# Performance work log

Hardware: AMD Instinct MI355X
Metric: run time of the kernel (lower is better)

Reference implementation:

```python
import jax, jax.numpy as jnp
import numpy as np

N = 50000      # nodes
E = 800000     # edges (avg degree 16)
IN = 128       # in_dim == hidden_dim*num_heads so residuals fire
D = 32         # hidden_dim (per-head)
H = 4          # num_heads
OUT = 64       # out_dim (final layer has 1 head)
NEG_SLOPE = 0.2
LN_EPS = 1e-5


def setup_inputs() -> dict:
    key = jax.random.key(0)
    ks = jax.random.split(key, 16)
    rn = lambda k, s: jax.random.normal(k, s, jnp.float32) * 0.05
    return {
        "features": jax.random.normal(ks[0], (N, IN), jnp.float32),
        "edge_weight": jax.random.uniform(ks[1], (E,), jnp.float32),
        "src": jax.random.randint(ks[2], (E,), 0, N),
        "dst": jax.random.randint(ks[3], (E,), 0, N),
        "W0": rn(ks[4], (IN, H * D)), "al0": rn(ks[5], (H, D)), "ar0": rn(ks[6], (H, D)), "lam0": jnp.float32(1.0),
        "W1": rn(ks[7], (H * D, H * D)), "al1": rn(ks[8], (H, D)), "ar1": rn(ks[9], (H, D)), "lam1": jnp.float32(1.0),
        "W2": rn(ks[10], (H * D, OUT)), "al2": rn(ks[11], (1, OUT)), "ar2": rn(ks[12], (1, OUT)), "lam2": jnp.float32(1.0),
        "g0": jnp.ones((H * D,), jnp.float32), "b0": jnp.zeros((H * D,), jnp.float32),
        "g1": jnp.ones((H * D,), jnp.float32), "b1": jnp.zeros((H * D,), jnp.float32),
    }


def _gat_layer(h, W, al, ar, lam, src, dst, ew):
    n = h.shape[0]
    heads, d = al.shape
    ft = (h @ W).reshape(n, heads, d)                      # [N,H,D]
    el = jnp.sum(ft * al[None], axis=-1)                   # [N,H]
    er = jnp.sum(ft * ar[None], axis=-1)                   # [N,H]
    e = el[src] + er[dst] + lam * ew[:, None]              # [E,H] u_add_v + weight bias
    e = jax.nn.leaky_relu(e, NEG_SLOPE)
    # edge softmax over incoming edges of each dst node
    m = jax.ops.segment_max(e, dst, num_segments=n)        # [N,H]
    ex = jnp.exp(e - m[dst])
    s = jax.ops.segment_sum(ex, dst, num_segments=n)       # [N,H]
    a = ex / s[dst]                                        # [E,H]
    # u_mul_e + sum aggregation
    msg = ft[src] * a[:, :, None]                          # [E,H,D]
    return jax.ops.segment_sum(msg, dst, num_segments=n)   # [N,H,D]


def _layer_norm(x, g, b):
    mu = jnp.mean(x, axis=-1, keepdims=True)
    var = jnp.mean((x - mu) ** 2, axis=-1, keepdims=True)
    return (x - mu) * jax.lax.rsqrt(var + LN_EPS) * g + b


def _forward(features, edge_weight, src, dst,
             W0, al0, ar0, lam0, W1, al1, ar1, lam1, W2, al2, ar2, lam2,
             g0, b0, g1, b1):
    n = features.shape[0]
    h = features
    # layer 0
    h1 = _gat_layer(h, W0, al0, ar0, lam0, src, dst, edge_weight)
    h1 = jax.nn.elu(h1).reshape(n, -1)
    h1 = _layer_norm(h1, g0, b0)
    if h1.shape == h.shape:
        h1 = h1 + h
    # layer 1
    h2 = _gat_layer(h1, W1, al1, ar1, lam1, src, dst, edge_weight)
    h2 = jax.nn.elu(h2).reshape(n, -1)
    h2 = _layer_norm(h2, g1, b1)
    h2 = h2 + h1
    # layer 2 (single head, no activation)
    out = _gat_layer(h2, W2, al2, ar2, lam2, src, dst, edge_weight).reshape(n, -1)
    return out


def reference(features, edge_weight, src, dst,
              W0, al0, ar0, lam0, W1, al1, ar1, lam1, W2, al2, ar2, lam2,
              g0, b0, g1, b1):
    # eval mode: dropout off and _add_noise is identity, so noisy == clean
    h_clean = _forward(features, edge_weight, src, dst,
                       W0, al0, ar0, lam0, W1, al1, ar1, lam1, W2, al2, ar2, lam2,
                       g0, b0, g1, b1)
    return (h_clean, h_clean)
```

## Files before the change

kernel.cpp:

```cpp
#include <hip/hip_runtime.h>

#define NEG_SLOPE 0.2f
#define LN_EPS 1e-5f

typedef __attribute__((ext_vector_type(8))) short bf16x8;
typedef __attribute__((ext_vector_type(4))) float f32x4;

__device__ inline unsigned short f2bf(float f) {
    unsigned u = __float_as_uint(f);
    unsigned r = u + 0x7FFFu + ((u >> 16) & 1u);
    return (unsigned short)(r >> 16);
}

__device__ inline void unpack8(uint4 u, float* f) {
    f[0] = __uint_as_float(u.x << 16);
    f[1] = __uint_as_float(u.x & 0xFFFF0000u);
    f[2] = __uint_as_float(u.y << 16);
    f[3] = __uint_as_float(u.y & 0xFFFF0000u);
    f[4] = __uint_as_float(u.z << 16);
    f[5] = __uint_as_float(u.z & 0xFFFF0000u);
    f[6] = __uint_as_float(u.w << 16);
    f[7] = __uint_as_float(u.w & 0xFFFF0000u);
}


__global__ __launch_bounds__(256) void zero_wt_kernel(
    uint4* __restrict__ z, int nz, int ZB,
    const float* __restrict__ W0, const float* __restrict__ W1,
    const float* __restrict__ W2, unsigned short* __restrict__ Wt0,
    unsigned short* __restrict__ Wt1, unsigned short* __restrict__ Wt2) {
    int bid = blockIdx.x;
    if (bid < ZB) {
        int base = bid * 1024 + threadIdx.x;
        #pragma unroll
        for (int j = 0; j < 4; ++j) {
            int idx = base + j * 256;
            if (idx < nz) z[idx] = make_uint4(0, 0, 0, 0);
        }
    } else {
        int row = (bid - ZB) * 2 + (threadIdx.x >> 7);
        int k = threadIdx.x & 127;
        if (row < 128) {
            Wt0[row * 128 + k] = f2bf(W0[k * 128 + row]);
        } else if (row < 256) {
            int c = row - 128;
            Wt1[c * 128 + k] = f2bf(W1[k * 128 + c]);
        } else {
            int c = row - 256;
            Wt2[c * 128 + k] = f2bf(W2[k * 64 + c]);
        }
    }
}


__global__ __launch_bounds__(256) void hist_gemm0(
    const int* __restrict__ dst, int* __restrict__ counts, int* __restrict__ rank,
    int E, int RB, const float* __restrict__ Ap, const unsigned short* __restrict__ Wt,
    const float* __restrict__ al, const float* __restrict__ ar,
    unsigned short* __restrict__ ftb, float* __restrict__ el,
    float* __restrict__ er, int n) {
    constexpr int LDA = 136;
    constexpr int NT = 8, H = 4, D = 32;
    __shared__ unsigned short As[64 * LDA];
    __shared__ unsigned short Ws[NT * 16 * LDA];
    int t = threadIdx.x;
    if (blockIdx.x < RB) {
        int i = blockIdx.x * 256 + t;
        if (i < E) rank[i] = atomicAdd(&counts[dst[i] * 16], 1);
        return;
    }
    int row0 = (blockIdx.x - RB) * 64;

    const float4* A4 = (const float4*)Ap;
    #pragma unroll
    for (int j = 0; j < 8; ++j) {
        int idx = t + j * 256;
        int r = idx >> 5;
        int c4 = idx & 31;
        int row = row0 + r;
        float4 v = (row < n) ? A4[(size_t)row * 32 + c4] : make_float4(0.f, 0.f, 0.f, 0.f);
        unsigned p0 = (unsigned)f2bf(v.x) | ((unsigned)f2bf(v.y) << 16);
        unsigned p1 = (unsigned)f2bf(v.z) | ((unsigned)f2bf(v.w) << 16);
        *(uint2*)&As[r * LDA + c4 * 4] = make_uint2(p0, p1);
    }
    const uint4* Wg = (const uint4*)Wt;
    #pragma unroll
    for (int j = 0; j < NT; ++j) {
        int idx = t + j * 256;
        int r = idx >> 4;
        int c8 = idx & 15;
        *(uint4*)&Ws[r * LDA + c8 * 8] = Wg[idx];
    }
    __syncthreads();

    int w = t >> 6, lane = t & 63;
    int m = lane & 15, q = lane >> 4;
    f32x4 acc[NT] = {};
    const unsigned short* ap = &As[(w * 16 + m) * LDA + q * 8];
    #pragma unroll
    for (int kk = 0; kk < 4; ++kk) {
        bf16x8 a = *(const bf16x8*)(ap + kk * 32);
        #pragma unroll
        for (int nt = 0; nt < NT; ++nt) {
            bf16x8 b = *(const bf16x8*)&Ws[(nt * 16 + m) * LDA + kk * 32 + q * 8];
            acc[nt] = __builtin_amdgcn_mfma_f32_16x16x32_bf16(a, b, acc[nt], 0, 0, 0);
        }
    }

    float alv[NT], arv[NT];
    #pragma unroll
    for (int nt = 0; nt < NT; ++nt) {
        alv[nt] = al[nt * 16 + m];
        arv[nt] = ar[nt * 16 + m];
    }

    int orow = row0 + w * 16 + q * 4;
    #pragma unroll
    for (int r = 0; r < 4; ++r) {
        int row = orow + r;
        float pl[H] = {}, pr[H] = {};
        #pragma unroll
        for (int nt = 0; nt < NT; ++nt) {
            int h = (nt * 16) / D;
            pl[h] = fmaf(acc[nt][r], alv[nt], pl[h]);
            pr[h] = fmaf(acc[nt][r], arv[nt], pr[h]);
        }
        #pragma unroll
        for (int off = 1; off < 16; off <<= 1) {
            #pragma unroll
            for (int h = 0; h < H; ++h) {
                pl[h] += __shfl_xor(pl[h], off, 64);
                pr[h] += __shfl_xor(pr[h], off, 64);
            }
        }
        if (row < n) {
            #pragma unroll
            for (int nt = 0; nt < NT; ++nt)
                ftb[(size_t)row * 128 + nt * 16 + m] = f2bf(acc[nt][r]);
            if (m < H) {
                float vl = pl[0], vr = pr[0];
                #pragma unroll
                for (int h = 1; h < H; ++h)
                    if (m == h) { vl = pl[h]; vr = pr[h]; }
                el[row * H + m] = vl;
                er[row * H + m] = vr;
            }
        }
    }
}


__global__ __launch_bounds__(256) void scan1_kernel(const int* __restrict__ counts,
                                                    int* __restrict__ bsum,
                                                    int* __restrict__ dhist, int n) {
    __shared__ int lds[256];
    __shared__ int hbin[64];
    int t = threadIdx.x;
    if (t < 64) hbin[t] = 0;
    int i = blockIdx.x * 256 + t;
    int c = (i < n) ? counts[i * 16] : 0;
    lds[t] = c;
    __syncthreads();
    if (i < n) atomicAdd(&hbin[63 - (c < 63 ? c : 63)], 1);
    for (int off = 128; off > 0; off >>= 1) {
        int v = (t < off) ? lds[t + off] : 0;
        __syncthreads();
        if (t < off) lds[t] += v;
        __syncthreads();
    }
    if (t == 0) bsum[blockIdx.x] = lds[0];
    if (t < 64) {
        int h = hbin[t];
        if (h) atomicAdd(&dhist[t], h);
    }
}


__global__ __launch_bounds__(256) void scan3_kernel(const int* __restrict__ counts,
                                                    const int* __restrict__ bsum,
                                                    int* __restrict__ rowptr,
                                                    const int* __restrict__ dhist,
                                                    int* __restrict__ dbase,
                                                    int n, int E, int nscan) {
    __shared__ int lds[256];
    int t = threadIdx.x;
    lds[t] = (t < nscan) ? bsum[t] : 0;
    __syncthreads();
    for (int off = 1; off < 256; off <<= 1) {
        int v = (t >= off) ? lds[t - off] : 0;
        __syncthreads();
        lds[t] += v;
        __syncthreads();
    }
    int boff = (blockIdx.x > 0) ? lds[blockIdx.x - 1] : 0;
    __syncthreads();
    int i = blockIdx.x * 256 + t;
    int c = (i < n) ? counts[i * 16] : 0;
    lds[t] = c;
    __syncthreads();
    for (int off = 1; off < 256; off <<= 1) {
        int v = (t >= off) ? lds[t - off] : 0;
        __syncthreads();
        lds[t] += v;
        __syncthreads();
    }
    if (i < n) rowptr[i] = boff + lds[t] - c;
    if (i == n) rowptr[n] = E;
    if (blockIdx.x == 0 && t < 64) {
        int v = dhist[t];
        int x = v;
        #pragma unroll
        for (int off = 1; off < 64; off <<= 1) {
            int u = __shfl_up(x, off, 64);
            if (t >= off) x += u;
        }
        dbase[t] = x - v;
    }
}


__global__ __launch_bounds__(256) void place_kernel(
    const int* __restrict__ src, const int* __restrict__ dst,
    const float* __restrict__ ew, const int* __restrict__ rowptr,
    const int* __restrict__ rank, unsigned* __restrict__ edge_p,
    const int* __restrict__ dbase, int* __restrict__ dcount,
    int* __restrict__ perm, int E, int EB, int N) {
    __shared__ int lbin[64];
    __shared__ int lbase[64];
    int bid = blockIdx.x;
    int t = threadIdx.x;
    if (bid < EB) {
        int i = bid * 256 + t;
        if (i < E) {
            int p = rowptr[dst[i]] + rank[i];
            edge_p[p] = ((unsigned)f2bf(ew[i]) << 16) | (unsigned)src[i];
        }
    } else {
        if (t < 64) lbin[t] = 0;
        __syncthreads();
        int nidx = (bid - EB) * 256 + t;
        bool valid = nidx < N;
        int key = 0, myoff = 0;
        if (valid) {
            int deg = rowptr[nidx + 1] - rowptr[nidx];
            key = 63 - (deg < 63 ? deg : 63);
            myoff = atomicAdd(&lbin[key], 1);
        }
        __syncthreads();
        if (t < 64) lbase[t] = lbin[t] ? atomicAdd(&dcount[t], lbin[t]) : 0;
        __syncthreads();
        if (valid) perm[dbase[key] + lbase[key] + myoff] = nidx;
    }
}


__device__ inline void accum8(float* ax, uint4 u, float p) {
    ax[0] = fmaf(p, __uint_as_float(u.x << 16), ax[0]);
    ax[1] = fmaf(p, __uint_as_float(u.x & 0xFFFF0000u), ax[1]);
    ax[2] = fmaf(p, __uint_as_float(u.y << 16), ax[2]);
    ax[3] = fmaf(p, __uint_as_float(u.y & 0xFFFF0000u), ax[3]);
    ax[4] = fmaf(p, __uint_as_float(u.z << 16), ax[4]);
    ax[5] = fmaf(p, __uint_as_float(u.z & 0xFFFF0000u), ax[5]);
    ax[6] = fmaf(p, __uint_as_float(u.w << 16), ax[6]);
    ax[7] = fmaf(p, __uint_as_float(u.w & 0xFFFF0000u), ax[7]);
}

__device__ inline void accum4(float* ax, uint2 u, float p) {
    ax[0] = fmaf(p, __uint_as_float(u.x << 16), ax[0]);
    ax[1] = fmaf(p, __uint_as_float(u.x & 0xFFFF0000u), ax[1]);
    ax[2] = fmaf(p, __uint_as_float(u.y << 16), ax[2]);
    ax[3] = fmaf(p, __uint_as_float(u.y & 0xFFFF0000u), ax[3]);
}

template <int K>
__device__ inline void agg_batch(const uint4* __restrict__ ftb4,
                                 const float* __restrict__ el, unsigned ev, int j,
                                 int li, int head, float erv, float lam, float* ax,
                                 float& s) {
    unsigned ee[K];
    uint4 uu[K];
    float ll[K];
    #pragma unroll
    for (int k = 0; k < K; ++k) ee[k] = __shfl(ev, j + k, 16);
    #pragma unroll
    for (int k = 0; k < K; ++k) {
        unsigned sn = ee[k] & 0xFFFFu;
        uu[k] = ftb4[(size_t)sn * 16 + li];
        ll[k] = el[sn * 4 + head];
    }
    #pragma unroll
    for (int k = 0; k < K; ++k) {
        float v = ll[k] + erv + lam * __uint_as_float(ee[k] & 0xFFFF0000u);
        v = fmaxf(v, NEG_SLOPE * v);
        float p = __expf(v);
        accum8(ax, uu[k], p);
        s += p;
    }
}

template <int K>
__device__ inline void agg_batch_out(const uint2* __restrict__ ftb2,
                                     const float* __restrict__ el, unsigned ev,
                                     int j, int li, float erv, float lam, float* ax,
                                     float& s) {
    unsigned ee[K];
    uint2 uu[K];
    float ll[K];
    #pragma unroll
    for (int k = 0; k < K; ++k) ee[k] = __shfl(ev, j + k, 16);
    #pragma unroll
    for (int k = 0; k < K; ++k) {
        unsigned sn = ee[k] & 0xFFFFu;
        uu[k] = ftb2[(size_t)sn * 16 + li];
        ll[k] = el[sn];
    }
    #pragma unroll
    for (int k = 0; k < K; ++k) {
        float v = ll[k] + erv + lam * __uint_as_float(ee[k] & 0xFFFF0000u);
        v = fmaxf(v, NEG_SLOPE * v);
        float p = __expf(v);
        accum4(ax, uu[k], p);
        s += p;
    }
}


template <bool PREV32, int VER>
__global__ __launch_bounds__(256) void fused_agg_gemm(
    const int* __restrict__ rowptr, const unsigned* __restrict__ edge_p,
    const int* __restrict__ perm, const uint4* __restrict__ ftb4,
    const float* __restrict__ el_in, const float* __restrict__ er_in,
    const float* __restrict__ lam_p, const float* __restrict__ g,
    const float* __restrict__ b, const void* __restrict__ prevp,
    uint4* __restrict__ houtb, const unsigned short* __restrict__ Wt,
    const float* __restrict__ al, const float* __restrict__ ar,
    unsigned short* __restrict__ ftb_out, float* __restrict__ el_out,
    float* __restrict__ er_out, int n) {
    constexpr int LDA = 136;
    __shared__ unsigned short As[16 * LDA];
    __shared__ float red[2][4][16];
    int t = threadIdx.x;
    int node0 = blockIdx.x * 16;
    int nl = t >> 4;
    int gid = node0 + nl;
    int li = t & 15;

    if (gid < n) {
        int node = perm[gid];
        int head = li >> 2;
        float lam = lam_p[0];
        float erv = er_in[node * 4 + head];
        int s0 = rowptr[node], s1 = rowptr[node + 1];
        float ax[8] = {};
        float s = 0.f;

        for (int base = s0; base < s1; base += 16) {
            int m = s1 - base;
            if (m > 16) m = 16;
            unsigned ev = (li < m) ? edge_p[base + li] : 0u;
            int j = 0;
            for (; j + 8 <= m; j += 8)
                agg_batch<8>(ftb4, el_in, ev, j, li, head, erv, lam, ax, s);
            if (j + 4 <= m) {
                agg_batch<4>(ftb4, el_in, ev, j, li, head, erv, lam, ax, s);
                j += 4;
            }
            for (; j < m; ++j)
                agg_batch<1>(ftb4, el_in, ev, j, li, head, erv, lam, ax, s);
        }

        float inv = (s > 0.f) ? 1.f / s : 0.f;
        float x[8];
        float sum = 0.f, sq = 0.f;
        #pragma unroll
        for (int d = 0; d < 8; ++d) {
            float v = ax[d] * inv;
            v = (v > 0.f) ? v : expm1f(v);
            x[d] = v;
            sum += v;
            sq += v * v;
        }
        #pragma unroll
        for (int off = 1; off < 16; off <<= 1) {
            sum += __shfl_xor(sum, off, 16);
            sq += __shfl_xor(sq, off, 16);
        }
        float mu = sum * (1.f / 128.f);
        float var = sq * (1.f / 128.f) - mu * mu;
        float rs = rsqrtf(var + LN_EPS);

        const float4* g4 = (const float4*)g;
        const float4* b4 = (const float4*)b;
        float pv[8];
        if constexpr (PREV32) {
            const float4* p4 = (const float4*)prevp;
            #pragma unroll
            for (int h = 0; h < 2; ++h) {
                float4 v = p4[(size_t)node * 32 + li * 2 + h];
                pv[h * 4 + 0] = v.x; pv[h * 4 + 1] = v.y;
                pv[h * 4 + 2] = v.z; pv[h * 4 + 3] = v.w;
            }
        } else {
            unpack8(((const uint4*)prevp)[(size_t)node * 16 + li], pv);
        }
        float y[8];
        #pragma unroll
        for (int h = 0; h < 2; ++h) {
            float4 gv = g4[li * 2 + h];
            float4 bv = b4[li * 2 + h];
            y[h * 4 + 0] = (x[h * 4 + 0] - mu) * rs * gv.x + bv.x + pv[h * 4 + 0];
            y[h * 4 + 1] = (x[h * 4 + 1] - mu) * rs * gv.y + bv.y + pv[h * 4 + 1];
            y[h * 4 + 2] = (x[h * 4 + 2] - mu) * rs * gv.z + bv.z + pv[h * 4 + 2];
            y[h * 4 + 3] = (x[h * 4 + 3] - mu) * rs * gv.w + bv.w + pv[h * 4 + 3];
        }
        uint4 o;
        o.x = (unsigned)f2bf(y[0]) | ((unsigned)f2bf(y[1]) << 16);
        o.y = (unsigned)f2bf(y[2]) | ((unsigned)f2bf(y[3]) << 16);
        o.z = (unsigned)f2bf(y[4]) | ((unsigned)f2bf(y[5]) << 16);
        o.w = (unsigned)f2bf(y[6]) | ((unsigned)f2bf(y[7]) << 16);
        if constexpr (VER == 1) houtb[(size_t)node * 16 + li] = o;
        *(uint4*)&As[nl * LDA + li * 8] = o;
    } else {
        *(uint4*)&As[nl * LDA + li * 8] = make_uint4(0, 0, 0, 0);
    }
    __syncthreads();

    int w = t >> 6, lane = t & 63;
    int m = lane & 15, q = lane >> 4;
    if constexpr (VER == 1) {
        f32x4 acc[2] = {};
        #pragma unroll
        for (int kk = 0; kk < 4; ++kk) {
            bf16x8 a = *(const bf16x8*)&As[m * LDA + kk * 32 + q * 8];
            #pragma unroll
            for (int nt = 0; nt < 2; ++nt) {
                int col = w * 32 + nt * 16 + m;
                bf16x8 bb = *(const bf16x8*)&Wt[(size_t)col * 128 + kk * 32 + q * 8];
                acc[nt] = __builtin_amdgcn_mfma_f32_16x16x32_bf16(a, bb, acc[nt], 0, 0, 0);
            }
        }
        float alv0 = al[w * 32 + m], alv1 = al[w * 32 + 16 + m];
        float arv0 = ar[w * 32 + m], arv1 = ar[w * 32 + 16 + m];
        #pragma unroll
        for (int r = 0; r < 4; ++r) {
            int gr = node0 + q * 4 + r;
            float pl = acc[0][r] * alv0 + acc[1][r] * alv1;
            float pr = acc[0][r] * arv0 + acc[1][r] * arv1;
            #pragma unroll
            for (int off = 1; off < 16; off <<= 1) {
                pl += __shfl_xor(pl, off, 64);
                pr += __shfl_xor(pr, off, 64);
            }
            if (gr < n) {
                int row = perm[gr];
                ftb_out[(size_t)row * 128 + w * 32 + m] = f2bf(acc[0][r]);
                ftb_out[(size_t)row * 128 + w * 32 + 16 + m] = f2bf(acc[1][r]);
                if (m == 0) {
                    el_out[row * 4 + w] = pl;
                    er_out[row * 4 + w] = pr;
                }
            }
        }
    } else {
        f32x4 acc = {};
        #pragma unroll
        for (int kk = 0; kk < 4; ++kk) {
            bf16x8 a = *(const bf16x8*)&As[m * LDA + kk * 32 + q * 8];
            int col = w * 16 + m;
            bf16x8 bb = *(const bf16x8*)&Wt[(size_t)col * 128 + kk * 32 + q * 8];
            acc = __builtin_amdgcn_mfma_f32_16x16x32_bf16(a, bb, acc, 0, 0, 0);
        }
        float alv = al[w * 16 + m], arv = ar[w * 16 + m];
        #pragma unroll
        for (int r = 0; r < 4; ++r) {
            int gr = node0 + q * 4 + r;
            float pl = acc[r] * alv;
            float pr = acc[r] * arv;
            #pragma unroll
            for (int off = 1; off < 16; off <<= 1) {
                pl += __shfl_xor(pl, off, 64);
                pr += __shfl_xor(pr, off, 64);
            }
            if (gr < n) ftb_out[(size_t)perm[gr] * 64 + w * 16 + m] = f2bf(acc[r]);
            if (m == 0) {
                red[0][w][q * 4 + r] = pl;
                red[1][w][q * 4 + r] = pr;
            }
        }
        __syncthreads();
        if (t < 16) {
            int gr = node0 + t;
            if (gr < n) {
                int row = perm[gr];
                el_out[row] = red[0][0][t] + red[0][1][t] + red[0][2][t] + red[0][3][t];
                er_out[row] = red[1][0][t] + red[1][1][t] + red[1][2][t] + red[1][3][t];
            }
        }
    }
}


__global__ __launch_bounds__(256) void gat_agg_out(
    const int* __restrict__ rowptr, const unsigned* __restrict__ edge_p,
    const int* __restrict__ perm, const uint2* __restrict__ ftb2,
    const float* __restrict__ el, const float* __restrict__ er,
    const float* __restrict__ lam_p, float* __restrict__ out, int n) {
    int gid = blockIdx.x * 16 + (threadIdx.x >> 4);
    if (gid >= n) return;
    int node = perm[gid];
    int li = threadIdx.x & 15;
    float lam = lam_p[0];
    float erv = er[node];
    int s0 = rowptr[node], s1 = rowptr[node + 1];
    float ax[4] = {};
    float s = 0.f;

    for (int base = s0; base < s1; base += 16) {
        int m = s1 - base;
        if (m > 16) m = 16;
        unsigned ev = (li < m) ? edge_p[base + li] : 0u;
        int j = 0;
        for (; j + 8 <= m; j += 8)
            agg_batch_out<8>(ftb2, el, ev, j, li, erv, lam, ax, s);
        if (j + 4 <= m) {
            agg_batch_out<4>(ftb2, el, ev, j, li, erv, lam, ax, s);
            j += 4;
        }
        for (; j < m; ++j)
            agg_batch_out<1>(ftb2, el, ev, j, li, erv, lam, ax, s);
    }

    float inv = (s > 0.f) ? 1.f / s : 0.f;
    float4 y;
    y.x = ax[0] * inv;
    y.y = ax[1] * inv;
    y.z = ax[2] * inv;
    y.w = ax[3] * inv;
    ((float4*)out)[(size_t)node * 16 + li] = y;
    ((float4*)out)[(size_t)(n + node) * 16 + li] = y;
}


extern "C" void kernel_launch(void* const* d_in, const int* in_sizes, int n_in,
                              void* d_out, int out_size, void* d_ws, size_t ws_size,
                              hipStream_t stream) {
    const float* features = (const float*)d_in[0];
    const float* edge_weight = (const float*)d_in[1];
    const int* src = (const int*)d_in[2];
    const int* dst = (const int*)d_in[3];
    const float* W0 = (const float*)d_in[4];
    const float* al0 = (const float*)d_in[5];
    const float* ar0 = (const float*)d_in[6];
    const float* lam0 = (const float*)d_in[7];
    const float* W1 = (const float*)d_in[8];
    const float* al1 = (const float*)d_in[9];
    const float* ar1 = (const float*)d_in[10];
    const float* lam1 = (const float*)d_in[11];
    const float* W2 = (const float*)d_in[12];
    const float* al2 = (const float*)d_in[13];
    const float* ar2 = (const float*)d_in[14];
    const float* lam2 = (const float*)d_in[15];
    const float* g0 = (const float*)d_in[16];
    const float* b0 = (const float*)d_in[17];
    const float* g1 = (const float*)d_in[18];
    const float* b1 = (const float*)d_in[19];

    const int N = in_sizes[0] / 128;
    const int E = in_sizes[1];

    char* w = (char*)d_ws;
    size_t o = 0;
    auto carve = [&](size_t bytes) {
        char* p = w + o;
        o += (bytes + 255) & ~(size_t)255;
        return p;
    };
    int* counts = (int*)carve((size_t)N * 64);
    int* dhist = (int*)carve(256);
    int* dcount = (int*)carve(256);
    int* rowptr = (int*)carve((size_t)(N + 1) * 4);
    int* bsum = (int*)carve(256 * 4);
    int* dbase = (int*)carve(256);
    int* rank = (int*)carve((size_t)E * 4);
    unsigned* edge_p = (unsigned*)carve((size_t)E * 4);
    int* perm = (int*)carve((size_t)N * 4);
    unsigned short* ftbA = (unsigned short*)carve((size_t)N * 128 * 2);
    unsigned short* ftbB = (unsigned short*)carve((size_t)N * 128 * 2);
    unsigned short* ftbC = (unsigned short*)carve((size_t)N * 64 * 2);
    unsigned short* h1 = (unsigned short*)carve((size_t)N * 128 * 2);
    float* elA = (float*)carve((size_t)N * 4 * 4);
    float* erA = (float*)carve((size_t)N * 4 * 4);
    float* elB = (float*)carve((size_t)N * 4 * 4);
    float* erB = (float*)carve((size_t)N * 4 * 4);
    float* elC = (float*)carve((size_t)N * 4);
    float* erC = (float*)carve((size_t)N * 4);
    unsigned short* Wt0 = (unsigned short*)carve(128 * 128 * 2);
    unsigned short* Wt1 = (unsigned short*)carve(128 * 128 * 2);
    unsigned short* Wt2 = (unsigned short*)carve(64 * 128 * 2);

    const int nscan = (N + 255) / 256;
    const int ngemm = (N + 63) / 64;
    const int nagg = (N + 15) / 16;
    const int RB = (E + 255) / 256;
    const int nz = N * 4 + 32;
    const int ZB = (nz + 1023) / 1024;

    zero_wt_kernel<<<ZB + 160, 256, 0, stream>>>((uint4*)counts, nz, ZB,
                                                 W0, W1, W2, Wt0, Wt1, Wt2);
    hist_gemm0<<<RB + ngemm, 256, 0, stream>>>(dst, counts, rank, E, RB,
                                               features, Wt0, al0, ar0,
                                               ftbA, elA, erA, N);
    scan1_kernel<<<nscan, 256, 0, stream>>>(counts, bsum, dhist, N);
    scan3_kernel<<<(N + 1 + 255) / 256, 256, 0, stream>>>(counts, bsum, rowptr,
                                                          dhist, dbase, N, E, nscan);
    place_kernel<<<RB + nscan, 256, 0, stream>>>(src, dst, edge_weight, rowptr, rank,
                                                 edge_p, dbase, dcount, perm, E, RB, N);
    fused_agg_gemm<true, 1><<<nagg, 256, 0, stream>>>(
        rowptr, edge_p, perm, (const uint4*)ftbA, elA, erA, lam0, g0, b0, features,
        (uint4*)h1, Wt1, al1, ar1, ftbB, elB, erB, N);
    fused_agg_gemm<false, 2><<<nagg, 256, 0, stream>>>(
        rowptr, edge_p, perm, (const uint4*)ftbB, elB, erB, lam1, g1, b1, h1,
        nullptr, Wt2, al2, ar2, ftbC, elC, erC, N);
    gat_agg_out<<<nagg, 256, 0, stream>>>(rowptr, edge_p, perm, (const uint2*)ftbC,
                                          elC, erC, lam2, (float*)d_out, N);
}
```

Measured before the change: 290.1 us.

## Store node features in degree-sorted order and coalesce GEMM output writes

```diff
diff --git a/kernel.cpp b/kernel.cpp
--- a/kernel.cpp
+++ b/kernel.cpp
@@ -24,21 +24,17 @@
 }
 
 
-__global__ __launch_bounds__(256) void zero_wt_kernel(
-    uint4* __restrict__ z, int nz, int ZB,
-    const float* __restrict__ W0, const float* __restrict__ W1,
+__global__ __launch_bounds__(256) void prep_kernel(
+    const int* __restrict__ dst, int* __restrict__ counts, int* __restrict__ rank,
+    int E, int RB, const float* __restrict__ W0, const float* __restrict__ W1,
     const float* __restrict__ W2, unsigned short* __restrict__ Wt0,
     unsigned short* __restrict__ Wt1, unsigned short* __restrict__ Wt2) {
     int bid = blockIdx.x;
-    if (bid < ZB) {
-        int base = bid * 1024 + threadIdx.x;
-        #pragma unroll
-        for (int j = 0; j < 4; ++j) {
-            int idx = base + j * 256;
-            if (idx < nz) z[idx] = make_uint4(0, 0, 0, 0);
-        }
+    if (bid < RB) {
+        int i = bid * 256 + threadIdx.x;
+        if (i < E) rank[i] = atomicAdd(&counts[dst[i] * 16], 1);
     } else {
-        int row = (bid - ZB) * 2 + (threadIdx.x >> 7);
+        int row = (bid - RB) * 2 + (threadIdx.x >> 7);
         int k = threadIdx.x & 127;
         if (row < 128) {
             Wt0[row * 128 + k] = f2bf(W0[k * 128 + row]);
@@ -53,12 +49,101 @@
 }
 
 
-__global__ __launch_bounds__(256) void hist_gemm0(
-    const int* __restrict__ dst, int* __restrict__ counts, int* __restrict__ rank,
-    int E, int RB, const float* __restrict__ Ap, const unsigned short* __restrict__ Wt,
-    const float* __restrict__ al, const float* __restrict__ ar,
-    unsigned short* __restrict__ ftb, float* __restrict__ el,
-    float* __restrict__ er, int n) {
+__global__ __launch_bounds__(256) void scan1_kernel(const int* __restrict__ counts,
+                                                    int* __restrict__ bsum,
+                                                    int* __restrict__ dhist, int n) {
+    __shared__ int lds[256];
+    __shared__ int hbin[64];
+    int t = threadIdx.x;
+    if (t < 64) hbin[t] = 0;
+    int i = blockIdx.x * 256 + t;
+    int c = (i < n) ? counts[i * 16] : 0;
+    lds[t] = c;
+    __syncthreads();
+    if (i < n) atomicAdd(&hbin[63 - (c < 63 ? c : 63)], 1);
+    for (int off = 128; off > 0; off >>= 1) {
+        int v = (t < off) ? lds[t + off] : 0;
+        __syncthreads();
+        if (t < off) lds[t] += v;
+        __syncthreads();
+    }
+    if (t == 0) bsum[blockIdx.x] = lds[0];
+    if (t < 64) {
+        int h = hbin[t];
+        if (h) atomicAdd(&dhist[t], h);
+    }
+}
+
+
+__global__ __launch_bounds__(256) void scan3_kernel(
+    const int* __restrict__ counts, const int* __restrict__ bsum,
+    int* __restrict__ rowptr, const int* __restrict__ dhist,
+    int* __restrict__ dcount, int* __restrict__ perm, int* __restrict__ ipos,
+    int n, int E, int nscan) {
+    __shared__ int lds[256];
+    __shared__ int lbin[64];
+    __shared__ int lbase[64];
+    __shared__ int dbs[64];
+    int t = threadIdx.x;
+    if (t < 64) lbin[t] = 0;
+    lds[t] = (t < nscan) ? bsum[t] : 0;
+    __syncthreads();
+    for (int off = 1; off < 256; off <<= 1) {
+        int v = (t >= off) ? lds[t - off] : 0;
+        __syncthreads();
+        lds[t] += v;
+        __syncthreads();
+    }
+    int boff = (blockIdx.x > 0) ? lds[blockIdx.x - 1] : 0;
+    __syncthreads();
+    int i = blockIdx.x * 256 + t;
+    int c = (i < n) ? counts[i * 16] : 0;
+    lds[t] = c;
+    __syncthreads();
+    for (int off = 1; off < 256; off <<= 1) {
+        int v = (t >= off) ? lds[t - off] : 0;
+        __syncthreads();
+        lds[t] += v;
+        __syncthreads();
+    }
+    if (i < n) rowptr[i] = boff + lds[t] - c;
+    if (i == n) rowptr[n] = E;
+    int key = 0, off2 = 0;
+    bool valid = i < n;
+    if (valid) {
+        key = 63 - (c < 63 ? c : 63);
+        off2 = atomicAdd(&lbin[key], 1);
+    }
+    __syncthreads();
+    if (t < 64) {
+        int v = dhist[t];
+        int x = v;
+        #pragma unroll
+        for (int o = 1; o < 64; o <<= 1) {
+            int u = __shfl_up(x, o, 64);
+            if (t >= o) x += u;
+        }
+        dbs[t] = x - v;
+        lbase[t] = lbin[t] ? atomicAdd(&dcount[t], lbin[t]) : 0;
+    }
+    __syncthreads();
+    if (valid) {
+        int slot = dbs[key] + lbase[key] + off2;
+        perm[slot] = i;
+        ipos[i] = slot;
+    }
+}
+
+
+__global__ __launch_bounds__(256) void place_gemm0(
+    const int* __restrict__ src, const int* __restrict__ dst,
+    const float* __restrict__ ew, const int* __restrict__ rowptr,
+    const int* __restrict__ rank, const int* __restrict__ ipos,
+    unsigned* __restrict__ edge_p, int E, int RB,
+    const float* __restrict__ Ap, const int* __restrict__ perm,
+    const unsigned short* __restrict__ Wt, const float* __restrict__ al,
+    const float* __restrict__ ar, unsigned short* __restrict__ ftb,
+    float* __restrict__ el, float* __restrict__ er, int n) {
     constexpr int LDA = 136;
     constexpr int NT = 8, H = 4, D = 32;
     __shared__ unsigned short As[64 * LDA];
@@ -66,7 +151,10 @@
     int t = threadIdx.x;
     if (blockIdx.x < RB) {
         int i = blockIdx.x * 256 + t;
-        if (i < E) rank[i] = atomicAdd(&counts[dst[i] * 16], 1);
+        if (i < E) {
+            int p = rowptr[dst[i]] + rank[i];
+            edge_p[p] = ((unsigned)f2bf(ew[i]) << 16) | (unsigned)ipos[src[i]];
+        }
         return;
     }
     int row0 = (blockIdx.x - RB) * 64;
@@ -77,8 +165,9 @@
         int idx = t + j * 256;
         int r = idx >> 5;
         int c4 = idx & 31;
-        int row = row0 + r;
-        float4 v = (row < n) ? A4[(size_t)row * 32 + c4] : make_float4(0.f, 0.f, 0.f, 0.f);
+        int grow = row0 + r;
+        float4 v = make_float4(0.f, 0.f, 0.f, 0.f);
+        if (grow < n) v = A4[(size_t)perm[grow] * 32 + c4];
         unsigned p0 = (unsigned)f2bf(v.x) | ((unsigned)f2bf(v.y) << 16);
         unsigned p1 = (unsigned)f2bf(v.z) | ((unsigned)f2bf(v.w) << 16);
         *(uint2*)&As[r * LDA + c4 * 4] = make_uint2(p0, p1);
@@ -146,110 +235,6 @@
                 er[row * H + m] = vr;
             }
         }
-    }
-}
-
-
-__global__ __launch_bounds__(256) void scan1_kernel(const int* __restrict__ counts,
-                                                    int* __restrict__ bsum,
-                                                    int* __restrict__ dhist, int n) {
-    __shared__ int lds[256];
-    __shared__ int hbin[64];
-    int t = threadIdx.x;
-    if (t < 64) hbin[t] = 0;
-    int i = blockIdx.x * 256 + t;
-    int c = (i < n) ? counts[i * 16] : 0;
-    lds[t] = c;
-    __syncthreads();
-    if (i < n) atomicAdd(&hbin[63 - (c < 63 ? c : 63)], 1);
-    for (int off = 128; off > 0; off >>= 1) {
-        int v = (t < off) ? lds[t + off] : 0;
-        __syncthreads();
-        if (t < off) lds[t] += v;
-        __syncthreads();
-    }
-    if (t == 0) bsum[blockIdx.x] = lds[0];
-    if (t < 64) {
-        int h = hbin[t];
-        if (h) atomicAdd(&dhist[t], h);
-    }
-}
-
-
-__global__ __launch_bounds__(256) void scan3_kernel(const int* __restrict__ counts,
-                                                    const int* __restrict__ bsum,
-                                                    int* __restrict__ rowptr,
-                                                    const int* __restrict__ dhist,
-                                                    int* __restrict__ dbase,
-                                                    int n, int E, int nscan) {
-    __shared__ int lds[256];
-    int t = threadIdx.x;
-    lds[t] = (t < nscan) ? bsum[t] : 0;
-    __syncthreads();
-    for (int off = 1; off < 256; off <<= 1) {
-        int v = (t >= off) ? lds[t - off] : 0;
-        __syncthreads();
-        lds[t] += v;
-        __syncthreads();
-    }
-    int boff = (blockIdx.x > 0) ? lds[blockIdx.x - 1] : 0;
-    __syncthreads();
-    int i = blockIdx.x * 256 + t;
-    int c = (i < n) ? counts[i * 16] : 0;
-    lds[t] = c;
-    __syncthreads();
-    for (int off = 1; off < 256; off <<= 1) {
-        int v = (t >= off) ? lds[t - off] : 0;
-        __syncthreads();
-        lds[t] += v;
-        __syncthreads();
-    }
-    if (i < n) rowptr[i] = boff + lds[t] - c;
-    if (i == n) rowptr[n] = E;
-    if (blockIdx.x == 0 && t < 64) {
-        int v = dhist[t];
-        int x = v;
-        #pragma unroll
-        for (int off = 1; off < 64; off <<= 1) {
-            int u = __shfl_up(x, off, 64);
-            if (t >= off) x += u;
-        }
-        dbase[t] = x - v;
-    }
-}
-
-
-__global__ __launch_bounds__(256) void place_kernel(
-    const int* __restrict__ src, const int* __restrict__ dst,
-    const float* __restrict__ ew, const int* __restrict__ rowptr,
-    const int* __restrict__ rank, unsigned* __restrict__ edge_p,
-    const int* __restrict__ dbase, int* __restrict__ dcount,
-    int* __restrict__ perm, int E, int EB, int N) {
-    __shared__ int lbin[64];
-    __shared__ int lbase[64];
-    int bid = blockIdx.x;
-    int t = threadIdx.x;
-    if (bid < EB) {
-        int i = bid * 256 + t;
-        if (i < E) {
-            int p = rowptr[dst[i]] + rank[i];
-            edge_p[p] = ((unsigned)f2bf(ew[i]) << 16) | (unsigned)src[i];
-        }
-    } else {
-        if (t < 64) lbin[t] = 0;
-        __syncthreads();
-        int nidx = (bid - EB) * 256 + t;
-        bool valid = nidx < N;
-        int key = 0, myoff = 0;
-        if (valid) {
-            int deg = rowptr[nidx + 1] - rowptr[nidx];
-            key = 63 - (deg < 63 ? deg : 63);
-            myoff = atomicAdd(&lbin[key], 1);
-        }
-        __syncthreads();
-        if (t < 64) lbase[t] = lbin[t] ? atomicAdd(&dcount[t], lbin[t]) : 0;
-        __syncthreads();
-        if (valid) perm[dbase[key] + lbase[key] + myoff] = nidx;
     }
 }
 
@@ -346,11 +331,11 @@
     int li = t & 15;
 
     if (gid < n) {
-        int node = perm[gid];
         int head = li >> 2;
         float lam = lam_p[0];
-        float erv = er_in[node * 4 + head];
-        int s0 = rowptr[node], s1 = rowptr[node + 1];
+        float erv = er_in[gid * 4 + head];
+        int tnode = perm[gid];
+        int s0 = rowptr[tnode], s1 = rowptr[tnode + 1];
         float ax[8] = {};
         float s = 0.f;
 
@@ -396,12 +381,12 @@
             const float4* p4 = (const float4*)prevp;
             #pragma unroll
             for (int h = 0; h < 2; ++h) {
-                float4 v = p4[(size_t)node * 32 + li * 2 + h];
+                float4 v = p4[(size_t)tnode * 32 + li * 2 + h];
                 pv[h * 4 + 0] = v.x; pv[h * 4 + 1] = v.y;
                 pv[h * 4 + 2] = v.z; pv[h * 4 + 3] = v.w;
             }
         } else {
-            unpack8(((const uint4*)prevp)[(size_t)node * 16 + li], pv);
+            unpack8(((const uint4*)prevp)[(size_t)gid * 16 + li], pv);
         }
         float y[8];
         #pragma unroll
@@ -418,7 +403,7 @@
         o.y = (unsigned)f2bf(y[2]) | ((unsigned)f2bf(y[3]) << 16);
         o.z = (unsigned)f2bf(y[4]) | ((unsigned)f2bf(y[5]) << 16);
         o.w = (unsigned)f2bf(y[6]) | ((unsigned)f2bf(y[7]) << 16);
-        if constexpr (VER == 1) houtb[(size_t)node * 16 + li] = o;
+        if constexpr (VER == 1) houtb[(size_t)gid * 16 + li] = o;
         *(uint4*)&As[nl * LDA + li * 8] = o;
     } else {
         *(uint4*)&As[nl * LDA + li * 8] = make_uint4(0, 0, 0, 0);
@@ -443,7 +428,8 @@
         float arv0 = ar[w * 32 + m], arv1 = ar[w * 32 + 16 + m];
         #pragma unroll
         for (int r = 0; r < 4; ++r) {
-            int gr = node0 + q * 4 + r;
+            int srow = q * 4 + r;
+            int gr = node0 + srow;
             float pl = acc[0][r] * alv0 + acc[1][r] * alv1;
             float pr = acc[0][r] * arv0 + acc[1][r] * arv1;
             #pragma unroll
@@ -451,15 +437,24 @@
                 pl += __shfl_xor(pl, off, 64);
                 pr += __shfl_xor(pr, off, 64);
             }
-            if (gr < n) {
-                int row = perm[gr];
-                ftb_out[(size_t)row * 128 + w * 32 + m] = f2bf(acc[0][r]);
-                ftb_out[(size_t)row * 128 + w * 32 + 16 + m] = f2bf(acc[1][r]);
-                if (m == 0) {
-                    el_out[row * 4 + w] = pl;
-                    er_out[row * 4 + w] = pr;
-                }
-            }
+            if (m == 0 && gr < n) {
+                el_out[gr * 4 + w] = pl;
+                er_out[gr * 4 + w] = pr;
+            }
+        }
+        __syncthreads();
+        #pragma unroll
+        for (int r = 0; r < 4; ++r) {
+            int srow = q * 4 + r;
+            As[srow * LDA + w * 32 + m] = f2bf(acc[0][r]);
+            As[srow * LDA + w * 32 + 16 + m] = f2bf(acc[1][r]);
+        }
+        __syncthreads();
+        {
+            int row = t >> 4, c8 = t & 15;
+            int gr = node0 + row;
+            if (gr < n)
+                ((uint4*)ftb_out)[(size_t)gr * 16 + c8] = *(const uint4*)&As[row * LDA + c8 * 8];
         }
     } else {
         f32x4 acc = {};
@@ -473,7 +468,7 @@
         float alv = al[w * 16 + m], arv = ar[w * 16 + m];
         #pragma unroll
         for (int r = 0; r < 4; ++r) {
-            int gr = node0 + q * 4 + r;
+            int srow = q * 4 + r;
             float pl = acc[r] * alv;
             float pr = acc[r] * arv;
             #pragma unroll
@@ -481,19 +476,29 @@
                 pl += __shfl_xor(pl, off, 64);
                 pr += __shfl_xor(pr, off, 64);
             }
-            if (gr < n) ftb_out[(size_t)perm[gr] * 64 + w * 16 + m] = f2bf(acc[r]);
             if (m == 0) {
-                red[0][w][q * 4 + r] = pl;
-                red[1][w][q * 4 + r] = pr;
-            }
-        }
-        __syncthreads();
+                red[0][w][srow] = pl;
+                red[1][w][srow] = pr;
+            }
+        }
+        __syncthreads();
+        #pragma unroll
+        for (int r = 0; r < 4; ++r) {
+            int srow = q * 4 + r;
+            As[srow * LDA + w * 16 + m] = f2bf(acc[r]);
+        }
+        __syncthreads();
+        if (t < 128) {
+            int row = t >> 3, c8 = t & 7;
+            int gr = node0 + row;
+            if (gr < n)
+                ((uint4*)ftb_out)[(size_t)gr * 8 + c8] = *(const uint4*)&As[row * LDA + c8 * 8];
+        }
         if (t < 16) {
             int gr = node0 + t;
             if (gr < n) {
-                int row = perm[gr];
-                el_out[row] = red[0][0][t] + red[0][1][t] + red[0][2][t] + red[0][3][t];
-                er_out[row] = red[1][0][t] + red[1][1][t] + red[1][2][t] + red[1][3][t];
+                el_out[gr] = red[0][0][t] + red[0][1][t] + red[0][2][t] + red[0][3][t];
+                er_out[gr] = red[1][0][t] + red[1][1][t] + red[1][2][t] + red[1][3][t];
             }
         }
     }
@@ -507,11 +512,11 @@
     const float* __restrict__ lam_p, float* __restrict__ out, int n) {
     int gid = blockIdx.x * 16 + (threadIdx.x >> 4);
     if (gid >= n) return;
-    int node = perm[gid];
+    int tnode = perm[gid];
     int li = threadIdx.x & 15;
     float lam = lam_p[0];
-    float erv = er[node];
-    int s0 = rowptr[node], s1 = rowptr[node + 1];
+    float erv = er[gid];
+    int s0 = rowptr[tnode], s1 = rowptr[tnode + 1];
     float ax[4] = {};
     float s = 0.f;
 
@@ -536,8 +541,8 @@
     y.y = ax[1] * inv;
     y.z = ax[2] * inv;
     y.w = ax[3] * inv;
-    ((float4*)out)[(size_t)node * 16 + li] = y;
-    ((float4*)out)[(size_t)(n + node) * 16 + li] = y;
+    ((float4*)out)[(size_t)tnode * 16 + li] = y;
+    ((float4*)out)[(size_t)(n + tnode) * 16 + li] = y;
 }
 
 
@@ -580,10 +585,10 @@
     int* dcount = (int*)carve(256);
     int* rowptr = (int*)carve((size_t)(N + 1) * 4);
     int* bsum = (int*)carve(256 * 4);
-    int* dbase = (int*)carve(256);
     int* rank = (int*)carve((size_t)E * 4);
     unsigned* edge_p = (unsigned*)carve((size_t)E * 4);
     int* perm = (int*)carve((size_t)N * 4);
+    int* ipos = (int*)carve((size_t)N * 4);
     unsigned short* ftbA = (unsigned short*)carve((size_t)N * 128 * 2);
     unsigned short* ftbB = (unsigned short*)carve((size_t)N * 128 * 2);
     unsigned short* ftbC = (unsigned short*)carve((size_t)N * 64 * 2);
@@ -602,19 +607,17 @@
     const int ngemm = (N + 63) / 64;
     const int nagg = (N + 15) / 16;
     const int RB = (E + 255) / 256;
-    const int nz = N * 4 + 32;
-    const int ZB = (nz + 1023) / 1024;
-
-    zero_wt_kernel<<<ZB + 160, 256, 0, stream>>>((uint4*)counts, nz, ZB,
-                                                 W0, W1, W2, Wt0, Wt1, Wt2);
-    hist_gemm0<<<RB + ngemm, 256, 0, stream>>>(dst, counts, rank, E, RB,
-                                               features, Wt0, al0, ar0,
-                                               ftbA, elA, erA, N);
+
+    hipMemsetAsync(counts, 0, (size_t)N * 64 + 512, stream);
+    prep_kernel<<<RB + 160, 256, 0, stream>>>(dst, counts, rank, E, RB,
+                                              W0, W1, W2, Wt0, Wt1, Wt2);
     scan1_kernel<<<nscan, 256, 0, stream>>>(counts, bsum, dhist, N);
-    scan3_kernel<<<(N + 1 + 255) / 256, 256, 0, stream>>>(counts, bsum, rowptr,
-                                                          dhist, dbase, N, E, nscan);
-    place_kernel<<<RB + nscan, 256, 0, stream>>>(src, dst, edge_weight, rowptr, rank,
-                                                 edge_p, dbase, dcount, perm, E, RB, N);
+    scan3_kernel<<<(N + 1 + 255) / 256, 256, 0, stream>>>(counts, bsum, rowptr, dhist,
+                                                          dcount, perm, ipos, N, E,
+                                                          nscan);
+    place_gemm0<<<RB + ngemm, 256, 0, stream>>>(src, dst, edge_weight, rowptr, rank,
+                                                ipos, edge_p, E, RB, features, perm,
+                                                Wt0, al0, ar0, ftbA, elA, erA, N);
     fused_agg_gemm<true, 1><<<nagg, 256, 0, stream>>>(
         rowptr, edge_p, perm, (const uint4*)ftbA, elA, erA, lam0, g0, b0, features,
         (uint4*)h1, Wt1, al1, ar1, ftbB, elB, erB, N);
```

New measurement: 291.9 us. Within noise of the previous version (+0.6%).
